# Kernel tuning notes

Measured on AMD Instinct MI355X. Metric: run time of the kernel, lower is better.

## Reference

```python
import jax, jax.numpy as jnp
import numpy as np

B = 1024
NUM_FEATURES = 800  # 10*10 grid * 8 channels
L1, L2, L3, NUM_CLASSES = 1024, 15, 32, 1
STRIDE = 10  # max(1, (96+2*1-3)//(10-1))
VIS_THRESH = 0.0


def setup_inputs() -> dict:
    key = jax.random.key(0)
    ks = jax.random.split(key, 9)
    images = jax.random.normal(ks[0], (B, 3, 96, 96), dtype=jnp.float32)
    conv_w = jax.random.normal(ks[1], (8, 3, 3, 3), dtype=jnp.float32) * 0.1
    ft_w = jax.random.normal(ks[2], (NUM_FEATURES, L1), dtype=jnp.float32) * 0.1
    ft_b = jnp.zeros((L1,), dtype=jnp.float32)
    w1 = jax.random.normal(ks[3], (L2, L1), dtype=jnp.float32) * (1.0 / np.sqrt(L1))
    b1 = jax.random.normal(ks[4], (L2,), dtype=jnp.float32) * 0.01
    w2 = jax.random.normal(ks[5], (L3, L2), dtype=jnp.float32) * (1.0 / np.sqrt(L2))
    b2 = jax.random.normal(ks[6], (L3,), dtype=jnp.float32) * 0.01
    w3 = jax.random.normal(ks[7], (NUM_CLASSES, L3), dtype=jnp.float32) * (1.0 / np.sqrt(L3))
    b3 = jax.random.normal(ks[8], (NUM_CLASSES,), dtype=jnp.float32) * 0.01
    return {"images": images, "conv_w": conv_w, "ft_w": ft_w, "ft_b": ft_b,
            "w1": w1, "b1": b1, "w2": w2, "b2": b2, "w3": w3, "b3": b3}


def reference(images, conv_w, ft_w, ft_b, w1, b1, w2, b2, w3, b3):
    # Conv2d(3->8, k=3, stride=10, pad=1, no bias): [B,3,96,96] -> [B,8,10,10]
    x = jax.lax.conv_general_dilated(
        images, conv_w, window_strides=(STRIDE, STRIDE),
        padding=((1, 1), (1, 1)),
        dimension_numbers=("NCHW", "OIHW", "NCHW"))
    x = jnp.clip(x, -1.0, 1.0)  # Hardtanh
    # training-mode soft binarization
    binary = jax.nn.sigmoid(10.0 * (x - VIS_THRESH))
    bflat = binary.reshape(binary.shape[0], -1)  # [B, 800]
    # _to_sparse_features keeps only entries > 0.5; FeatureTransformer then does
    # a ragged gather-scale-sum == masked dense matmul with the FT weights.
    vals = jnp.where(bflat > 0.5, bflat, 0.0)
    features = vals @ ft_w + ft_b  # [B, L1]
    l0 = jnp.clip(features, 0.0, 1.0)
    h = L1 // 2
    s0, s1 = l0[:, :h], l0[:, h:]
    l0c = jnp.concatenate([s0 * s1, s0], axis=1) * (127.0 / 128.0)  # [B, L1]
    # SimpleClassifier: Linear->ReLU->Linear->ReLU->Linear
    h1 = jax.nn.relu(l0c @ w1.T + b1)
    h2 = jax.nn.relu(h1 @ w2.T + b2)
    out = h2 @ w3.T + b3  # [B, NUM_CLASSES]
    return out
```

## Files before the change

kernel.cpp:

```cpp
#include <hip/hip_runtime.h>

typedef unsigned short u16;
typedef unsigned int   u32;
typedef __attribute__((ext_vector_type(8))) short short8;
typedef __attribute__((ext_vector_type(4))) float f32x4;

__device__ __forceinline__ u16 f2bf(float f) {
    union { float f; u32 i; } v; v.f = f;
    u32 x = v.i;
    return (u16)((x + 0x7fffu + ((x >> 16) & 1u)) >> 16);
}
__device__ __forceinline__ float bf2f(u16 u) {
    union { u32 i; float f; } v; v.i = ((u32)u) << 16; return v.f;
}

__global__ __launch_bounds__(256) void k1_fused(
    const float* __restrict__ images,
    const float* __restrict__ conv_w,
    const float* __restrict__ ft_w,
    u16* __restrict__ vh, u16* __restrict__ vl,
    u16* __restrict__ bth, u16* __restrict__ btl)
{
    __shared__ float img_s[3][29][100];
    __shared__ float w[216];
    __shared__ float tile[32][33];

    int t = threadIdx.x;

    if (blockIdx.x >= 1024) {
        int bid = blockIdx.x - 1024;
        int kb = bid / 32, nb = bid - kb * 32;
        int k0 = kb * 32, n0 = nb * 32;
        int tx = t & 31, ty = t >> 5;
        #pragma unroll
        for (int i = 0; i < 4; i++) {
            int k = ty + i * 8;
            tile[k][tx] = ft_w[(k0 + k) * 1024 + n0 + tx];
        }
        __syncthreads();
        #pragma unroll
        for (int i = 0; i < 4; i++) {
            int n = ty + i * 8;
            float wv = tile[tx][n];
            u16 hi = f2bf(wv);
            float lo = wv - bf2f(hi);
            bth[(n0 + n) * 800 + k0 + tx] = hi;
            btl[(n0 + n) * 800 + k0 + tx] = f2bf(lo);
        }
        return;
    }

    int b = blockIdx.x;
    if (t < 216) w[t] = conv_w[t];

    for (int i = t; i < 3 * 29 * 24; i += 256) {
        int ch  = i / (29 * 24);
        int rem = i - ch * (29 * 24);
        int lr  = rem / 24;
        int x4  = rem - lr * 24;
        int ih  = 10 * ((lr + 1) / 3) + (lr + 1) % 3 - 1;
        *(float4*)&img_s[ch][lr][x4 * 4] =
            *(const float4*)&images[((b * 3 + ch) * 96 + ih) * 96 + x4 * 4];
    }
    __syncthreads();

    for (int ridx = t; ridx < 800; ridx += 256) {
        int o  = ridx / 100;
        int p  = ridx - o * 100;
        int oh = p / 10;
        int ow = p - oh * 10;

        float sum = 0.0f;
        #pragma unroll
        for (int ic = 0; ic < 3; ic++) {
            const float* wc = &w[o * 27 + ic * 9];
            #pragma unroll
            for (int kh = 0; kh < 3; kh++) {
                int lr = 3 * oh + kh - 1;
                if (lr < 0) continue;
                #pragma unroll
                for (int kw = 0; kw < 3; kw++) {
                    int iw = ow * 10 + kw - 1;
                    if (iw < 0) continue;
                    sum = fmaf(img_s[ic][lr][iw], wc[kh * 3 + kw], sum);
                }
            }
        }
        float xc = fminf(fmaxf(sum, -1.0f), 1.0f);
        float binary = 1.0f / (1.0f + __expf(-10.0f * xc));
        float v = (binary > 0.5f) ? binary : 0.0f;
        u16 hi = f2bf(v);
        vh[b * 800 + ridx] = hi;
        vl[b * 800 + ridx] = f2bf(v - bf2f(hi));
    }
}

__global__ __launch_bounds__(256) void k2_mfma(
    const u16* __restrict__ Ah, const u16* __restrict__ Al,
    const u16* __restrict__ Bh, const u16* __restrict__ Bl,
    float* __restrict__ C0, float* __restrict__ C1)
{
    __shared__ u16 sAh[64 * 40], sAl[64 * 40], sBh[64 * 40], sBl[64 * 40];
    int t = threadIdx.x;
    int m0 = blockIdx.y * 64, n0 = blockIdx.x * 64;
    int kb = (blockIdx.z == 0) ? 0 : 416;
    int ke = (blockIdx.z == 0) ? 416 : 800;
    float* C = (blockIdx.z == 0) ? C0 : C1;

    int w = t >> 6, lane = t & 63;
    int quad = lane >> 4, lo4 = lane & 15;
    int wm = (w >> 1) * 32, wn = (w & 1) * 32;

    int sr = t >> 2;
    int sq = t & 3;
    const u16* gAh = Ah + (m0 + sr) * 800 + sq * 8;
    const u16* gAl = Al + (m0 + sr) * 800 + sq * 8;
    const u16* gBh = Bh + (n0 + sr) * 800 + sq * 8;
    const u16* gBl = Bl + (n0 + sr) * 800 + sq * 8;
    int sdst = sr * 40 + sq * 8;

    f32x4 acc[2][2] = {};

    uint4 rAh = *(const uint4*)(gAh + kb);
    uint4 rAl = *(const uint4*)(gAl + kb);
    uint4 rBh = *(const uint4*)(gBh + kb);
    uint4 rBl = *(const uint4*)(gBl + kb);

    for (int k0 = kb; k0 < ke; k0 += 32) {
        *(uint4*)&sAh[sdst] = rAh;
        *(uint4*)&sAl[sdst] = rAl;
        *(uint4*)&sBh[sdst] = rBh;
        *(uint4*)&sBl[sdst] = rBl;
        __syncthreads();

        if (k0 + 32 < ke) {
            rAh = *(const uint4*)(gAh + k0 + 32);
            rAl = *(const uint4*)(gAl + k0 + 32);
            rBh = *(const uint4*)(gBh + k0 + 32);
            rBl = *(const uint4*)(gBl + k0 + 32);
        }

        short8 a_h[2], a_l[2], b_h[2], b_l[2];
        #pragma unroll
        for (int f = 0; f < 2; f++) {
            int mi = (wm + f * 16 + lo4) * 40 + quad * 8;
            a_h[f] = *(const short8*)&sAh[mi];
            a_l[f] = *(const short8*)&sAl[mi];
            int ni = (wn + f * 16 + lo4) * 40 + quad * 8;
            b_h[f] = *(const short8*)&sBh[ni];
            b_l[f] = *(const short8*)&sBl[ni];
        }
        #pragma unroll
        for (int fm = 0; fm < 2; fm++)
            #pragma unroll
            for (int fn = 0; fn < 2; fn++) {
                acc[fm][fn] = __builtin_amdgcn_mfma_f32_16x16x32_bf16(a_h[fm], b_h[fn], acc[fm][fn], 0, 0, 0);
                acc[fm][fn] = __builtin_amdgcn_mfma_f32_16x16x32_bf16(a_h[fm], b_l[fn], acc[fm][fn], 0, 0, 0);
                acc[fm][fn] = __builtin_amdgcn_mfma_f32_16x16x32_bf16(a_l[fm], b_h[fn], acc[fm][fn], 0, 0, 0);
            }
        __syncthreads();
    }

    #pragma unroll
    for (int fm = 0; fm < 2; fm++) {
        #pragma unroll
        for (int fn = 0; fn < 2; fn++) {
            int n = n0 + wn + fn * 16 + lo4;
            #pragma unroll
            for (int r = 0; r < 4; r++) {
                int m = m0 + wm + fm * 16 + quad * 4 + r;
                C[m * 1024 + n] = acc[fm][fn][r];
            }
        }
    }
}

__global__ __launch_bounds__(256) void k3_tail(
    const float* __restrict__ l0a,
    const float* __restrict__ l0b,
    const float* __restrict__ ft_b,
    const float* __restrict__ w1,
    const float* __restrict__ b1,
    const float* __restrict__ w2,
    const float* __restrict__ b2,
    const float* __restrict__ w3,
    const float* __restrict__ b3,
    float* __restrict__ out)
{
    __shared__ float red[2][15];

    int wave = threadIdx.x >> 6;
    int lane = threadIdx.x & 63;
    int row  = wave >> 1;
    int half = wave & 1;
    int b = blockIdx.x * 2 + row;
    const float* pa = l0a + b * 1024;
    const float* pb = l0b + b * 1024;
    const float cc = 0.9921875f;

    float acc[15];
    #pragma unroll
    for (int j = 0; j < 15; j++) acc[j] = 0.f;

    {
        int k4 = (lane + half * 64) * 4;
        float4 a0 = *(const float4*)(pa + k4);
        float4 q0 = *(const float4*)(pb + k4);
        float4 f0 = *(const float4*)(ft_b + k4);
        float4 a1 = *(const float4*)(pa + k4 + 512);
        float4 q1 = *(const float4*)(pb + k4 + 512);
        float4 f1 = *(const float4*)(ft_b + k4 + 512);
        float4 x0, x1;
        x0.x = fminf(fmaxf(a0.x + q0.x + f0.x, 0.f), 1.f);
        x0.y = fminf(fmaxf(a0.y + q0.y + f0.y, 0.f), 1.f);
        x0.z = fminf(fmaxf(a0.z + q0.z + f0.z, 0.f), 1.f);
        x0.w = fminf(fmaxf(a0.w + q0.w + f0.w, 0.f), 1.f);
        x1.x = fminf(fmaxf(a1.x + q1.x + f1.x, 0.f), 1.f);
        x1.y = fminf(fmaxf(a1.y + q1.y + f1.y, 0.f), 1.f);
        x1.z = fminf(fmaxf(a1.z + q1.z + f1.z, 0.f), 1.f);
        x1.w = fminf(fmaxf(a1.w + q1.w + f1.w, 0.f), 1.f);

        float4 va, vb;
        va.x = x0.x * x1.x * cc; va.y = x0.y * x1.y * cc;
        va.z = x0.z * x1.z * cc; va.w = x0.w * x1.w * cc;
        vb.x = x0.x * cc; vb.y = x0.y * cc;
        vb.z = x0.z * cc; vb.w = x0.w * cc;
        #pragma unroll
        for (int j = 0; j < 15; j++) {
            float4 wa = *(const float4*)(w1 + j * 1024 + k4);
            float4 wb = *(const float4*)(w1 + j * 1024 + k4 + 512);
            acc[j] = fmaf(va.x, wa.x, acc[j]); acc[j] = fmaf(va.y, wa.y, acc[j]);
            acc[j] = fmaf(va.z, wa.z, acc[j]); acc[j] = fmaf(va.w, wa.w, acc[j]);
            acc[j] = fmaf(vb.x, wb.x, acc[j]); acc[j] = fmaf(vb.y, wb.y, acc[j]);
            acc[j] = fmaf(vb.z, wb.z, acc[j]); acc[j] = fmaf(vb.w, wb.w, acc[j]);
        }
    }

    #pragma unroll
    for (int j = 0; j < 15; j++) {
        #pragma unroll
        for (int m = 32; m >= 1; m >>= 1)
            acc[j] += __shfl_xor(acc[j], m, 64);
    }

    if (half == 1 && lane == 0) {
        #pragma unroll
        for (int j = 0; j < 15; j++) red[row][j] = acc[j];
    }
    __syncthreads();

    if (half == 0) {
        float h1[15];
        #pragma unroll
        for (int j = 0; j < 15; j++)
            h1[j] = fmaxf(acc[j] + red[row][j] + b1[j], 0.f);

        float contrib = 0.f;
        if (lane < 32) {
            float h2 = b2[lane];
            #pragma unroll
            for (int j = 0; j < 15; j++) h2 = fmaf(h1[j], w2[lane * 15 + j], h2);
            h2 = fmaxf(h2, 0.f);
            contrib = h2 * w3[lane];
        }
        #pragma unroll
        for (int m = 32; m >= 1; m >>= 1) contrib += __shfl_xor(contrib, m, 64);

        if (lane == 0) out[b] = contrib + b3[0];
    }
}

extern "C" void kernel_launch(void* const* d_in, const int* in_sizes, int n_in,
                              void* d_out, int out_size, void* d_ws, size_t ws_size,
                              hipStream_t stream) {
    const float* images = (const float*)d_in[0];
    const float* conv_w = (const float*)d_in[1];
    const float* ft_w   = (const float*)d_in[2];
    const float* ft_b   = (const float*)d_in[3];
    const float* w1     = (const float*)d_in[4];
    const float* b1     = (const float*)d_in[5];
    const float* w2     = (const float*)d_in[6];
    const float* b2     = (const float*)d_in[7];
    const float* w3     = (const float*)d_in[8];
    const float* b3     = (const float*)d_in[9];
    float* out = (float*)d_out;

    const int NV = 1024 * 800;
    u16* vh  = (u16*)d_ws;
    u16* vl  = vh + NV;
    u16* bth = vl + NV;
    u16* btl = bth + NV;
    float* l0a = (float*)(btl + NV);
    float* l0b = l0a + 1024 * 1024;

    k1_fused<<<1824, 256, 0, stream>>>(images, conv_w, ft_w, vh, vl, bth, btl);
    k2_mfma<<<dim3(16, 16, 2), 256, 0, stream>>>(vh, vl, bth, btl, l0a, l0b);
    k3_tail<<<512, 256, 0, stream>>>(l0a, l0b, ft_b, w1, b1, w2, b2, w3, b3, out);
}
```

Measured before the change: 190.6 us.

## Fuse split-K reduction and bias/clamp into GEMM; split conv blocks by half-image

```diff
diff --git a/kernel.cpp b/kernel.cpp
--- a/kernel.cpp
+++ b/kernel.cpp
@@ -21,14 +21,14 @@
     u16* __restrict__ vh, u16* __restrict__ vl,
     u16* __restrict__ bth, u16* __restrict__ btl)
 {
-    __shared__ float img_s[3][29][100];
+    __shared__ float img_s[3][15][100];
     __shared__ float w[216];
     __shared__ float tile[32][33];
 
     int t = threadIdx.x;
 
-    if (blockIdx.x >= 1024) {
-        int bid = blockIdx.x - 1024;
+    if (blockIdx.x >= 2048) {
+        int bid = blockIdx.x - 2048;
         int kb = bid / 32, nb = bid - kb * 32;
         int k0 = kb * 32, n0 = nb * 32;
         int tx = t & 31, ty = t >> 5;
@@ -50,25 +50,27 @@
         return;
     }
 
-    int b = blockIdx.x;
+    int b = blockIdx.x >> 1;
+    int h = blockIdx.x & 1;
     if (t < 216) w[t] = conv_w[t];
 
-    for (int i = t; i < 3 * 29 * 24; i += 256) {
-        int ch  = i / (29 * 24);
-        int rem = i - ch * (29 * 24);
-        int lr  = rem / 24;
-        int x4  = rem - lr * 24;
+    for (int i = t; i < 3 * 15 * 24; i += 256) {
+        int ch  = i / (15 * 24);
+        int rem = i - ch * (15 * 24);
+        int lrl = rem / 24;
+        int x4  = rem - lrl * 24;
+        int lr  = h * 14 + lrl;
         int ih  = 10 * ((lr + 1) / 3) + (lr + 1) % 3 - 1;
-        *(float4*)&img_s[ch][lr][x4 * 4] =
+        *(float4*)&img_s[ch][lrl][x4 * 4] =
             *(const float4*)&images[((b * 3 + ch) * 96 + ih) * 96 + x4 * 4];
     }
     __syncthreads();
 
-    for (int ridx = t; ridx < 800; ridx += 256) {
-        int o  = ridx / 100;
-        int p  = ridx - o * 100;
-        int oh = p / 10;
-        int ow = p - oh * 10;
+    for (int ridx = t; ridx < 400; ridx += 256) {
+        int o    = ridx / 50;
+        int p    = ridx - o * 50;
+        int oh_l = p / 10;
+        int ow   = p - oh_l * 10;
 
         float sum = 0.0f;
         #pragma unroll
@@ -76,13 +78,13 @@
             const float* wc = &w[o * 27 + ic * 9];
             #pragma unroll
             for (int kh = 0; kh < 3; kh++) {
-                int lr = 3 * oh + kh - 1;
-                if (lr < 0) continue;
+                int lrl = h + 3 * oh_l + kh - 1;
+                if (lrl < 0) continue;
                 #pragma unroll
                 for (int kw = 0; kw < 3; kw++) {
                     int iw = ow * 10 + kw - 1;
                     if (iw < 0) continue;
-                    sum = fmaf(img_s[ic][lr][iw], wc[kh * 3 + kw], sum);
+                    sum = fmaf(img_s[ic][lrl][iw], wc[kh * 3 + kw], sum);
                 }
             }
         }
@@ -90,35 +92,49 @@
         float binary = 1.0f / (1.0f + __expf(-10.0f * xc));
         float v = (binary > 0.5f) ? binary : 0.0f;
         u16 hi = f2bf(v);
-        vh[b * 800 + ridx] = hi;
-        vl[b * 800 + ridx] = f2bf(v - bf2f(hi));
-    }
-}
-
-__global__ __launch_bounds__(256) void k2_mfma(
+        int rg = o * 100 + (h * 5 + oh_l) * 10 + ow;
+        vh[b * 800 + rg] = hi;
+        vl[b * 800 + rg] = f2bf(v - bf2f(hi));
+    }
+}
+
+union KSmem {
+    struct { u16 Ah[2][64 * 40], Al[2][64 * 40], Bh[2][64 * 40], Bl[2][64 * 40]; } s;
+    float red[4][64][17];
+};
+
+__global__ __launch_bounds__(512) void k2_mfma(
     const u16* __restrict__ Ah, const u16* __restrict__ Al,
     const u16* __restrict__ Bh, const u16* __restrict__ Bl,
-    float* __restrict__ C0, float* __restrict__ C1)
+    const float* __restrict__ ft_b,
+    float* __restrict__ C)
 {
-    __shared__ u16 sAh[64 * 40], sAl[64 * 40], sBh[64 * 40], sBl[64 * 40];
+    __shared__ KSmem ks;
     int t = threadIdx.x;
     int m0 = blockIdx.y * 64, n0 = blockIdx.x * 64;
-    int kb = (blockIdx.z == 0) ? 0 : 416;
-    int ke = (blockIdx.z == 0) ? 416 : 800;
-    float* C = (blockIdx.z == 0) ? C0 : C1;
-
-    int w = t >> 6, lane = t & 63;
+
+    int wave = t >> 6;
+    int group = wave >> 2;
+    int w4 = wave & 3;
+    int lane = t & 63;
     int quad = lane >> 4, lo4 = lane & 15;
-    int wm = (w >> 1) * 32, wn = (w & 1) * 32;
-
-    int sr = t >> 2;
-    int sq = t & 3;
+    int wm = (w4 >> 1) * 32, wn = (w4 & 1) * 32;
+
+    int kb = group * 416;
+    int ke = group ? 800 : 416;
+
+    int tg = t & 255;
+    int sr = tg >> 2;
+    int sq = tg & 3;
     const u16* gAh = Ah + (m0 + sr) * 800 + sq * 8;
     const u16* gAl = Al + (m0 + sr) * 800 + sq * 8;
     const u16* gBh = Bh + (n0 + sr) * 800 + sq * 8;
     const u16* gBl = Bl + (n0 + sr) * 800 + sq * 8;
     int sdst = sr * 40 + sq * 8;
 
+    u16* sAh = ks.s.Ah[group]; u16* sAl = ks.s.Al[group];
+    u16* sBh = ks.s.Bh[group]; u16* sBl = ks.s.Bl[group];
+
     f32x4 acc[2][2] = {};
 
     uint4 rAh = *(const uint4*)(gAh + kb);
@@ -126,11 +142,15 @@
     uint4 rBh = *(const uint4*)(gBh + kb);
     uint4 rBl = *(const uint4*)(gBl + kb);
 
-    for (int k0 = kb; k0 < ke; k0 += 32) {
-        *(uint4*)&sAh[sdst] = rAh;
-        *(uint4*)&sAl[sdst] = rAl;
-        *(uint4*)&sBh[sdst] = rBh;
-        *(uint4*)&sBl[sdst] = rBl;
+    for (int i = 0; i < 13; i++) {
+        int k0 = kb + i * 32;
+        bool act = (k0 < ke);
+        if (act) {
+            *(uint4*)&sAh[sdst] = rAh;
+            *(uint4*)&sAl[sdst] = rAl;
+            *(uint4*)&sBh[sdst] = rBh;
+            *(uint4*)&sBl[sdst] = rBl;
+        }
         __syncthreads();
 
         if (k0 + 32 < ke) {
@@ -140,45 +160,62 @@
             rBl = *(const uint4*)(gBl + k0 + 32);
         }
 
-        short8 a_h[2], a_l[2], b_h[2], b_l[2];
-        #pragma unroll
-        for (int f = 0; f < 2; f++) {
-            int mi = (wm + f * 16 + lo4) * 40 + quad * 8;
-            a_h[f] = *(const short8*)&sAh[mi];
-            a_l[f] = *(const short8*)&sAl[mi];
-            int ni = (wn + f * 16 + lo4) * 40 + quad * 8;
-            b_h[f] = *(const short8*)&sBh[ni];
-            b_l[f] = *(const short8*)&sBl[ni];
-        }
+        if (act) {
+            short8 a_h[2], a_l[2], b_h[2], b_l[2];
+            #pragma unroll
+            for (int f = 0; f < 2; f++) {
+                int mi = (wm + f * 16 + lo4) * 40 + quad * 8;
+                a_h[f] = *(const short8*)&sAh[mi];
+                a_l[f] = *(const short8*)&sAl[mi];
+                int ni = (wn + f * 16 + lo4) * 40 + quad * 8;
+                b_h[f] = *(const short8*)&sBh[ni];
+                b_l[f] = *(const short8*)&sBl[ni];
+            }
+            #pragma unroll
+            for (int fm = 0; fm < 2; fm++)
+                #pragma unroll
+                for (int fn = 0; fn < 2; fn++) {
+                    acc[fm][fn] = __builtin_amdgcn_mfma_f32_16x16x32_bf16(a_h[fm], b_h[fn], acc[fm][fn], 0, 0, 0);
+                    acc[fm][fn] = __builtin_amdgcn_mfma_f32_16x16x32_bf16(a_h[fm], b_l[fn], acc[fm][fn], 0, 0, 0);
+                    acc[fm][fn] = __builtin_amdgcn_mfma_f32_16x16x32_bf16(a_l[fm], b_h[fn], acc[fm][fn], 0, 0, 0);
+                }
+        }
+        __syncthreads();
+    }
+
+    if (group == 1) {
+        float* rp = &ks.red[w4][lane][0];
         #pragma unroll
         for (int fm = 0; fm < 2; fm++)
             #pragma unroll
+            for (int fn = 0; fn < 2; fn++)
+                #pragma unroll
+                for (int r = 0; r < 4; r++)
+                    rp[(fm * 2 + fn) * 4 + r] = acc[fm][fn][r];
+    }
+    __syncthreads();
+
+    if (group == 0) {
+        const float* rp = &ks.red[w4][lane][0];
+        #pragma unroll
+        for (int fm = 0; fm < 2; fm++) {
+            #pragma unroll
             for (int fn = 0; fn < 2; fn++) {
-                acc[fm][fn] = __builtin_amdgcn_mfma_f32_16x16x32_bf16(a_h[fm], b_h[fn], acc[fm][fn], 0, 0, 0);
-                acc[fm][fn] = __builtin_amdgcn_mfma_f32_16x16x32_bf16(a_h[fm], b_l[fn], acc[fm][fn], 0, 0, 0);
-                acc[fm][fn] = __builtin_amdgcn_mfma_f32_16x16x32_bf16(a_l[fm], b_h[fn], acc[fm][fn], 0, 0, 0);
+                int n = n0 + wn + fn * 16 + lo4;
+                float bv = ft_b[n];
+                #pragma unroll
+                for (int r = 0; r < 4; r++) {
+                    int m = m0 + wm + fm * 16 + quad * 4 + r;
+                    float v = acc[fm][fn][r] + rp[(fm * 2 + fn) * 4 + r] + bv;
+                    C[m * 1024 + n] = fminf(fmaxf(v, 0.f), 1.f);
+                }
             }
-        __syncthreads();
-    }
-
-    #pragma unroll
-    for (int fm = 0; fm < 2; fm++) {
-        #pragma unroll
-        for (int fn = 0; fn < 2; fn++) {
-            int n = n0 + wn + fn * 16 + lo4;
-            #pragma unroll
-            for (int r = 0; r < 4; r++) {
-                int m = m0 + wm + fm * 16 + quad * 4 + r;
-                C[m * 1024 + n] = acc[fm][fn][r];
-            }
         }
     }
 }
 
 __global__ __launch_bounds__(256) void k3_tail(
-    const float* __restrict__ l0a,
-    const float* __restrict__ l0b,
-    const float* __restrict__ ft_b,
+    const float* __restrict__ l0,
     const float* __restrict__ w1,
     const float* __restrict__ b1,
     const float* __restrict__ w2,
@@ -194,8 +231,7 @@
     int row  = wave >> 1;
     int half = wave & 1;
     int b = blockIdx.x * 2 + row;
-    const float* pa = l0a + b * 1024;
-    const float* pb = l0b + b * 1024;
+    const float* rowp = l0 + b * 1024;
     const float cc = 0.9921875f;
 
     float acc[15];
@@ -204,21 +240,8 @@
 
     {
         int k4 = (lane + half * 64) * 4;
-        float4 a0 = *(const float4*)(pa + k4);
-        float4 q0 = *(const float4*)(pb + k4);
-        float4 f0 = *(const float4*)(ft_b + k4);
-        float4 a1 = *(const float4*)(pa + k4 + 512);
-        float4 q1 = *(const float4*)(pb + k4 + 512);
-        float4 f1 = *(const float4*)(ft_b + k4 + 512);
-        float4 x0, x1;
-        x0.x = fminf(fmaxf(a0.x + q0.x + f0.x, 0.f), 1.f);
-        x0.y = fminf(fmaxf(a0.y + q0.y + f0.y, 0.f), 1.f);
-        x0.z = fminf(fmaxf(a0.z + q0.z + f0.z, 0.f), 1.f);
-        x0.w = fminf(fmaxf(a0.w + q0.w + f0.w, 0.f), 1.f);
-        x1.x = fminf(fmaxf(a1.x + q1.x + f1.x, 0.f), 1.f);
-        x1.y = fminf(fmaxf(a1.y + q1.y + f1.y, 0.f), 1.f);
-        x1.z = fminf(fmaxf(a1.z + q1.z + f1.z, 0.f), 1.f);
-        x1.w = fminf(fmaxf(a1.w + q1.w + f1.w, 0.f), 1.f);
+        float4 x0 = *(const float4*)(rowp + k4);
+        float4 x1 = *(const float4*)(rowp + k4 + 512);
 
         float4 va, vb;
         va.x = x0.x * x1.x * cc; va.y = x0.y * x1.y * cc;
@@ -290,10 +313,9 @@
     u16* vl  = vh + NV;
     u16* bth = vl + NV;
     u16* btl = bth + NV;
-    float* l0a = (float*)(btl + NV);
-    float* l0b = l0a + 1024 * 1024;
-
-    k1_fused<<<1824, 256, 0, stream>>>(images, conv_w, ft_w, vh, vl, bth, btl);
-    k2_mfma<<<dim3(16, 16, 2), 256, 0, stream>>>(vh, vl, bth, btl, l0a, l0b);
-    k3_tail<<<512, 256, 0, stream>>>(l0a, l0b, ft_b, w1, b1, w2, b2, w3, b3, out);
-}
+    float* l0 = (float*)(btl + NV);
+
+    k1_fused<<<2848, 256, 0, stream>>>(images, conv_w, ft_w, vh, vl, bth, btl);
+    k2_mfma<<<dim3(16, 16), 512, 0, stream>>>(vh, vl, bth, btl, ft_b, l0);
+    k3_tail<<<512, 256, 0, stream>>>(l0, w1, b1, w2, b2, w3, b3, out);
+}
```

Measured after the change: 194.3 us. About the same (+1.9%).
